# Kernel tuning notes

Hardware: AMD Instinct MI355X
Metric: run time of the kernel (lower is better)

The kernel has to match this reference:

```python
import jax, jax.numpy as jnp
import numpy as np

HID = 256
POS_FREQ = 10
DIR_FREQ = 4
POS_ENC = 3 * (2 * POS_FREQ + 1)   # 63
DIR_ENC = 3 * (2 * DIR_FREQ + 1)   # 27
N_PTS = 262144


def _posenc(x, num_freq):
    freqs = (2.0 ** jnp.arange(num_freq)).astype(x.dtype)      # [F]
    xf = x[..., None, :] * freqs[:, None]                       # [..., F, D]
    sc = jnp.stack([jnp.sin(xf), jnp.cos(xf)], axis=-2)         # [..., F, 2, D]
    return jnp.concatenate([x, sc.reshape(*x.shape[:-1], -1)], axis=-1)


def _linear_init(key, fan_in, fan_out):
    kw, kb = jax.random.split(key)
    s = 1.0 / np.sqrt(fan_in)
    W = jax.random.uniform(kw, (fan_in, fan_out), jnp.float32, -s, s)
    b = jax.random.uniform(kb, (fan_out,), jnp.float32, -s, s)
    return W, b


def setup_inputs() -> dict:
    key = jax.random.key(0)
    ks = jax.random.split(key, 16)
    inp = {
        "positions": jax.random.normal(ks[0], (N_PTS, 3), jnp.float32),
        "directions": jax.random.normal(ks[1], (N_PTS, 3), jnp.float32),
    }
    W, b = _linear_init(ks[2], POS_ENC, HID)
    inp["W_in"], inp["b_in"] = W, b
    # 7 hidden layers; layer index 4 takes skip concat (HID + POS_ENC)
    for i in range(7):
        fan_in = HID + POS_ENC if i == 4 else HID
        W, b = _linear_init(ks[3 + i], fan_in, HID)
        inp[f"W_h{i}"], inp[f"b_h{i}"] = W, b
    W, b = _linear_init(ks[10], HID, HID + 1)
    inp["W_out"], inp["b_out"] = W, b
    W, b = _linear_init(ks[11], HID + DIR_ENC, HID // 2)
    inp["W_r1"], inp["b_r1"] = W, b
    W, b = _linear_init(ks[12], HID // 2, 3)
    inp["W_r2"], inp["b_r2"] = W, b
    return inp


def _forward(positions, directions, W_in, b_in, hidden_params, W_out, b_out,
             W_r1, b_r1, W_r2, b_r2):
    pe = _posenc(positions, POS_FREQ)    # [N, 63]
    de = _posenc(directions, DIR_FREQ)   # [N, 27]
    h = jax.nn.relu(pe @ W_in + b_in)    # [N, 256]
    for i, (W, b) in enumerate(hidden_params):
        if i == 4:
            h = jnp.concatenate([h, pe], axis=-1)  # skip connection [N, 319]
        h = jax.nn.relu(h @ W + b)
    out = h @ W_out + b_out                      # [N, 257]
    features = out[..., :HID]                    # [N, 256]
    density = jax.nn.relu(out[..., HID:HID + 1])  # [N, 1]
    rgb_in = jnp.concatenate([features, de], axis=-1)  # [N, 283]
    rgb = jax.nn.sigmoid(jax.nn.relu(rgb_in @ W_r1 + b_r1) @ W_r2 + b_r2)  # [N, 3]
    return rgb, density


def reference(positions, directions, W_in, b_in,
              W_h0, b_h0, W_h1, b_h1, W_h2, b_h2, W_h3, b_h3,
              W_h4, b_h4, W_h5, b_h5, W_h6, b_h6,
              W_out, b_out, W_r1, b_r1, W_r2, b_r2):
    hidden = [(W_h0, b_h0), (W_h1, b_h1), (W_h2, b_h2), (W_h3, b_h3),
              (W_h4, b_h4), (W_h5, b_h5), (W_h6, b_h6)]
    return _forward(positions, directions, W_in, b_in, hidden,
                    W_out, b_out, W_r1, b_r1, W_r2, b_r2)
```

## Files before the change

kernel.cpp:

```cpp
#include <hip/hip_runtime.h>
#include <math.h>

#define NPTS 262144
#define MT 128

typedef __attribute__((ext_vector_type(8))) short bf16x8;
typedef __attribute__((ext_vector_type(4))) float f32x4;
typedef __attribute__((ext_vector_type(16))) float f32x16;
typedef __attribute__((ext_vector_type(2))) unsigned int u32x2;

#if defined(__has_builtin)
#if __has_builtin(__builtin_amdgcn_cvt_pk_bf16_f32)
#define HAVE_CVT_PK_BF16 1
#endif
#endif

__device__ __forceinline__ short f2bf(float f) {
    union { float f; unsigned u; } v; v.f = f;
    unsigned r = v.u + 0x7fffu + ((v.u >> 16) & 1u);
    return (short)(r >> 16);
}
__device__ __forceinline__ unsigned pk2(float a, float b) {
#ifdef HAVE_CVT_PK_BF16
    auto r = __builtin_amdgcn_cvt_pk_bf16_f32(a, b);
    unsigned u; __builtin_memcpy(&u, &r, 4);
    return u;
#else
    return ((unsigned)(unsigned short)f2bf(a)) |
           ((unsigned)(unsigned short)f2bf(b) << 16);
#endif
}

__device__ __forceinline__ void barrier_lds() {
    asm volatile("s_waitcnt lgkmcnt(0)" ::: "memory");
    __builtin_amdgcn_s_barrier();
}

#define OFF_IN   0
#define SZ_IN    (64*256)
#define OFF_H0   (OFF_IN + SZ_IN)
#define SZ_H     (256*256)
#define OFF_H1   (OFF_H0 + SZ_H)
#define OFF_H2   (OFF_H1 + SZ_H)
#define OFF_H3   (OFF_H2 + SZ_H)
#define OFF_H4   (OFF_H3 + SZ_H)
#define SZ_H4    (320*256)
#define OFF_H5   (OFF_H4 + SZ_H4)
#define OFF_H6   (OFF_H5 + SZ_H)
#define OFF_OUT  (OFF_H6 + SZ_H)
#define SZ_OUTM  (256*256)
#define OFF_OUTD (OFF_OUT + SZ_OUTM)
#define SZ_OUTD  (256*16)
#define OFF_R1   (OFF_OUTD + SZ_OUTD)
#define SZ_R1    (288*128)
#define OFF_R2   (OFF_R1 + SZ_R1)
#define SZ_R2    (128*16)
#define WS_TOTAL (OFF_R2 + SZ_R2)

struct PrepP { const float* W[11]; short* ws; };

__global__ __launch_bounds__(256) void prep_all(PrepP pp) {
    int i = blockIdx.x * 256 + threadIdx.x;
    if (i >= WS_TOTAL) return;
    const int offs[13] = {OFF_IN, OFF_H0, OFF_H1, OFF_H2, OFF_H3, OFF_H4,
                          OFF_H5, OFF_H6, OFF_OUT, OFF_OUTD, OFF_R1, OFF_R2,
                          WS_TOTAL};
    const int wsrc[12] = {0,1,2,3,4,5,6,7,8,8,9,10};
    const int Ks[12]   = {63,256,256,256,256,319,256,256,256,256,283,128};
    const int Nsrc[12] = {256,256,256,256,256,256,256,256,257,257,128,3};
    int seg = 0;
    while (i >= offs[seg + 1]) seg++;
    int li = i - offs[seg];
    int j = li & 7, L = (li >> 3) & 63, tile = li >> 9;
    const float* W = pp.W[wsrc[seg]];
    float v = 0.f;
    if (seg == 9) {
        int k = tile * 32 + ((L >> 4) << 3) + j;
        if (k < 256 && (L & 15) == 0) v = W[k * 257 + 256];
    } else if (seg == 11) {
        int k = tile * 32 + ((L >> 4) << 3) + j;
        int n = L & 15;
        if (k < 128 && n < 3) v = W[k * 3 + n];
    } else {
        int nNb = (seg == 10) ? 4 : 8;
        int nb = tile % nNb, kt = tile / nNb;
        int k = kt * 16 + ((L >> 5) << 3) + j;
        int n = nb * 32 + (L & 31);
        if (k < Ks[seg]) v = W[k * Nsrc[seg] + n];
    }
    pp.ws[i] = f2bf(v);
}

struct Params {
    const float *pos, *dir;
    const float *b_in, *b_h0, *b_h1, *b_h2, *b_h3, *b_h4, *b_h5, *b_h6;
    const float *b_out, *b_r1, *b_r2;
    const short *w;
    float *out;
};

template<int NKT, int NNB, int NS, int TM, int MODE>
__device__ __forceinline__ void layer32(const short* __restrict__ Wsw,
                                        const short* __restrict__ Wd,
                                        const float* __restrict__ bias,
                                        short* X, float* dout, int p0,
                                        int nbB, int mbB, int wave, int lane) {
    const int l31 = lane & 31, hi = lane >> 5;
    const short* xb = X + hi * 1024 + (mbB * 32 + l31) * 8;
    const short* wp = Wsw + (size_t)(nbB * 64 + lane) * 8;

    bf16x8 a0[NS], a1[NS];
#pragma unroll
    for (int s = 0; s < NS; s++)
        a0[s] = *(const bf16x8*)(wp + (size_t)s * 512);
#pragma unroll
    for (int s = 0; s < NS; s++)
        a1[s] = *(const bf16x8*)(wp + (size_t)(NNB + s) * 512);

    barrier_lds();

    if (MODE == 1) {
        const int l15 = lane & 15, quad = lane >> 4;
        const short* xd = X + quad * 1024 + (wave * 16 + l15) * 8;
        f32x4 ad = (f32x4){0.f, 0.f, 0.f, 0.f};
#pragma unroll
        for (int kt = 0; kt < 8; ++kt) {
            bf16x8 b = *(const bf16x8*)(xd + kt * 4096);
            bf16x8 a = *(const bf16x8*)(Wd + (size_t)(kt * 64 + lane) * 8);
            ad = __builtin_amdgcn_mfma_f32_16x16x32_bf16(a, b, ad, 0, 0, 0);
        }
        if (quad == 0)
            dout[3 * NPTS + p0 + wave * 16 + l15] = fmaxf(ad[0] + bias[256], 0.f);
    }

    f32x16 acc[NS][TM];
#pragma unroll
    for (int s = 0; s < NS; s++)
#pragma unroll
        for (int t = 0; t < TM; t++)
#pragma unroll
            for (int r = 0; r < 16; r++) acc[s][t][r] = 0.f;

    bf16x8 b_c[TM];
#pragma unroll
    for (int t = 0; t < TM; t++)
        b_c[t] = *(const bf16x8*)(xb + t * 256);

#pragma unroll
    for (int kt = 0; kt < NKT; ++kt) {
        bf16x8 b_n[TM], a_n[NS];
        if (kt + 1 < NKT) {
#pragma unroll
            for (int t = 0; t < TM; t++)
                b_n[t] = *(const bf16x8*)(xb + (kt + 1) * 2048 + t * 256);
        }
        if (kt + 2 < NKT) {
#pragma unroll
            for (int s = 0; s < NS; s++)
                a_n[s] = *(const bf16x8*)(wp + (size_t)((kt + 2) * NNB + s) * 512);
        }
        if ((kt & 1) == 0) {
#pragma unroll
            for (int s = 0; s < NS; s++)
#pragma unroll
                for (int t = 0; t < TM; t++)
                    acc[s][t] = __builtin_amdgcn_mfma_f32_32x32x16_bf16(a0[s], b_c[t], acc[s][t], 0, 0, 0);
        } else {
#pragma unroll
            for (int s = 0; s < NS; s++)
#pragma unroll
                for (int t = 0; t < TM; t++)
                    acc[s][t] = __builtin_amdgcn_mfma_f32_32x32x16_bf16(a1[s], b_c[t], acc[s][t], 0, 0, 0);
        }
        if (kt + 2 < NKT) {
            if ((kt & 1) == 0) {
#pragma unroll
                for (int s = 0; s < NS; s++) a0[s] = a_n[s];
            } else {
#pragma unroll
                for (int s = 0; s < NS; s++) a1[s] = a_n[s];
            }
        }
        if (kt + 1 < NKT) {
#pragma unroll
            for (int t = 0; t < TM; t++) b_c[t] = b_n[t];
        }
    }

    barrier_lds();

#pragma unroll
    for (int s = 0; s < NS; s++) {
        const int nb = nbB + s;
#pragma unroll
        for (int t = 0; t < TM; t++) {
            const int m = (mbB + t) * 32 + l31;
#pragma unroll
            for (int rq = 0; rq < 4; rq++) {
                const int nbase = nb * 32 + rq * 8 + hi * 4;
                const f32x4 bv = *(const f32x4*)(bias + nbase);
                float v0 = acc[s][t][rq * 4 + 0] + bv[0];
                float v1 = acc[s][t][rq * 4 + 1] + bv[1];
                float v2 = acc[s][t][rq * 4 + 2] + bv[2];
                float v3 = acc[s][t][rq * 4 + 3] + bv[3];
                if (MODE == 0) {
                    v0 = fmaxf(v0, 0.f); v1 = fmaxf(v1, 0.f);
                    v2 = fmaxf(v2, 0.f); v3 = fmaxf(v3, 0.f);
                }
                u32x2 w; w[0] = pk2(v0, v1); w[1] = pk2(v2, v3);
                *(u32x2*)(X + (size_t)(nb * 4 + rq) * 1024 + m * 8 + hi * 4) = w;
            }
        }
    }
}

__global__ __launch_bounds__(512, 4) void nerf_fused(Params P) {
    __shared__ __align__(16) short X[40 * 1024];
    const int tid = threadIdx.x;
    const int wave = tid >> 6, lane = tid & 63;
    const int p0 = blockIdx.x * MT;

    const int nbB_h = (wave & 3) * 2, mbB_h = (wave >> 2) * 2;

    for (int i = tid; i < 128 * 8; i += 512) {
        const int pt = i & 127, g = i >> 7;
        const float x0 = P.pos[(p0 + pt) * 3 + 0];
        const float x1 = P.pos[(p0 + pt) * 3 + 1];
        const float x2 = P.pos[(p0 + pt) * 3 + 2];
        bf16x8 v;
#pragma unroll
        for (int j = 0; j < 8; j++) {
            const int d = g * 8 + j;
            float val = 0.f;
            if (d < 3) val = (d == 0) ? x0 : (d == 1) ? x1 : x2;
            else if (d < 63) {
                const int e = d - 3, f = e / 6, r = e % 6;
                const float x = (r % 3 == 0) ? x0 : (r % 3 == 1) ? x1 : x2;
                const float xf = x * (float)(1 << f);
                val = (r < 3) ? sinf(xf) : cosf(xf);
            }
            v[j] = f2bf(val);
        }
        *(bf16x8*)(X + ((size_t)g * 128 + pt) * 8) = v;
        *(bf16x8*)(X + ((size_t)(32 + g) * 128 + pt) * 8) = v;
    }

    layer32< 4, 8, 2, 2, 0>(P.w + OFF_IN, nullptr, P.b_in, X, P.out, p0, nbB_h, mbB_h, wave, lane);
    layer32<16, 8, 2, 2, 0>(P.w + OFF_H0, nullptr, P.b_h0, X, P.out, p0, nbB_h, mbB_h, wave, lane);
    layer32<16, 8, 2, 2, 0>(P.w + OFF_H1, nullptr, P.b_h1, X, P.out, p0, nbB_h, mbB_h, wave, lane);
    layer32<16, 8, 2, 2, 0>(P.w + OFF_H2, nullptr, P.b_h2, X, P.out, p0, nbB_h, mbB_h, wave, lane);
    layer32<16, 8, 2, 2, 0>(P.w + OFF_H3, nullptr, P.b_h3, X, P.out, p0, nbB_h, mbB_h, wave, lane);
    layer32<20, 8, 2, 2, 0>(P.w + OFF_H4, nullptr, P.b_h4, X, P.out, p0, nbB_h, mbB_h, wave, lane);

    {
        const int ptD = tid & 127, gD = tid >> 7;
        const float x0 = P.dir[(p0 + ptD) * 3 + 0];
        const float x1 = P.dir[(p0 + ptD) * 3 + 1];
        const float x2 = P.dir[(p0 + ptD) * 3 + 2];
        bf16x8 de_v;
#pragma unroll
        for (int j = 0; j < 8; j++) {
            const int d = gD * 8 + j;
            float val = 0.f;
            if (d < 3) val = (d == 0) ? x0 : (d == 1) ? x1 : x2;
            else if (d < 27) {
                const int e = d - 3, f = e / 6, r = e % 6;
                const float x = (r % 3 == 0) ? x0 : (r % 3 == 1) ? x1 : x2;
                const float xf = x * (float)(1 << f);
                val = (r < 3) ? sinf(xf) : cosf(xf);
            }
            de_v[j] = f2bf(val);
        }
        *(bf16x8*)(X + ((size_t)(32 + gD) * 128 + ptD) * 8) = de_v;
    }

    layer32<16, 8, 2, 2, 0>(P.w + OFF_H5, nullptr, P.b_h5, X, P.out, p0, nbB_h, mbB_h, wave, lane);
    layer32<16, 8, 2, 2, 0>(P.w + OFF_H6, nullptr, P.b_h6, X, P.out, p0, nbB_h, mbB_h, wave, lane);
    layer32<16, 8, 2, 2, 1>(P.w + OFF_OUT, P.w + OFF_OUTD, P.b_out, X, P.out, p0, nbB_h, mbB_h, wave, lane);

    layer32<18, 4, 2, 1, 0>(P.w + OFF_R1, nullptr, P.b_r1, X, P.out, p0, (wave & 1) * 2, wave >> 1, wave, lane);

    barrier_lds();
    {
        const int l15 = lane & 15, quad = lane >> 4;
        const short* xb = X + quad * 1024 + (wave * 16 + l15) * 8;
        bf16x8 a0 = *(const bf16x8*)(P.w + OFF_R2 + (size_t)(0 * 64 + lane) * 8);
        bf16x8 a1 = *(const bf16x8*)(P.w + OFF_R2 + (size_t)(1 * 64 + lane) * 8);
        bf16x8 a2 = *(const bf16x8*)(P.w + OFF_R2 + (size_t)(2 * 64 + lane) * 8);
        bf16x8 a3 = *(const bf16x8*)(P.w + OFF_R2 + (size_t)(3 * 64 + lane) * 8);
        f32x4 acc = (f32x4){0.f, 0.f, 0.f, 0.f};
        bf16x8 b0 = *(const bf16x8*)(xb);
        bf16x8 b1 = *(const bf16x8*)(xb + 4096);
        bf16x8 b2 = *(const bf16x8*)(xb + 8192);
        bf16x8 b3 = *(const bf16x8*)(xb + 12288);
        acc = __builtin_amdgcn_mfma_f32_16x16x32_bf16(a0, b0, acc, 0, 0, 0);
        acc = __builtin_amdgcn_mfma_f32_16x16x32_bf16(a1, b1, acc, 0, 0, 0);
        acc = __builtin_amdgcn_mfma_f32_16x16x32_bf16(a2, b2, acc, 0, 0, 0);
        acc = __builtin_amdgcn_mfma_f32_16x16x32_bf16(a3, b3, acc, 0, 0, 0);
        if (quad == 0) {
#pragma unroll
            for (int r = 0; r < 3; r++) {
                const float v = acc[r] + P.b_r2[r];
                P.out[(size_t)(p0 + wave * 16 + l15) * 3 + r] = 1.f / (1.f + expf(-v));
            }
        }
    }
}

extern "C" void kernel_launch(void* const* d_in, const int* in_sizes, int n_in,
                              void* d_out, int out_size, void* d_ws, size_t ws_size,
                              hipStream_t stream) {
    short* ws = (short*)d_ws;

    PrepP pp;
    pp.W[0]  = (const float*)d_in[2];
    pp.W[1]  = (const float*)d_in[4];
    pp.W[2]  = (const float*)d_in[6];
    pp.W[3]  = (const float*)d_in[8];
    pp.W[4]  = (const float*)d_in[10];
    pp.W[5]  = (const float*)d_in[12];
    pp.W[6]  = (const float*)d_in[14];
    pp.W[7]  = (const float*)d_in[16];
    pp.W[8]  = (const float*)d_in[18];
    pp.W[9]  = (const float*)d_in[20];
    pp.W[10] = (const float*)d_in[22];
    pp.ws = ws;
    hipLaunchKernelGGL(prep_all, dim3((WS_TOTAL + 255) / 256), dim3(256), 0, stream, pp);

    Params P;
    P.pos  = (const float*)d_in[0];
    P.dir  = (const float*)d_in[1];
    P.b_in = (const float*)d_in[3];
    P.b_h0 = (const float*)d_in[5];
    P.b_h1 = (const float*)d_in[7];
    P.b_h2 = (const float*)d_in[9];
    P.b_h3 = (const float*)d_in[11];
    P.b_h4 = (const float*)d_in[13];
    P.b_h5 = (const float*)d_in[15];
    P.b_h6 = (const float*)d_in[17];
    P.b_out = (const float*)d_in[19];
    P.b_r1 = (const float*)d_in[21];
    P.b_r2 = (const float*)d_in[23];
    P.w = ws;
    P.out = (float*)d_out;
    hipLaunchKernelGGL(nerf_fused, dim3(NPTS / MT), dim3(512), 0, stream, P);
}
```

Baseline: 416.8 us.

## Halve block to 4 waves with each wave covering all 128 rows

```diff
diff --git a/kernel.cpp b/kernel.cpp
--- a/kernel.cpp
+++ b/kernel.cpp
@@ -121,16 +121,20 @@
 
     if (MODE == 1) {
         const int l15 = lane & 15, quad = lane >> 4;
-        const short* xd = X + quad * 1024 + (wave * 16 + l15) * 8;
-        f32x4 ad = (f32x4){0.f, 0.f, 0.f, 0.f};
-#pragma unroll
-        for (int kt = 0; kt < 8; ++kt) {
-            bf16x8 b = *(const bf16x8*)(xd + kt * 4096);
-            bf16x8 a = *(const bf16x8*)(Wd + (size_t)(kt * 64 + lane) * 8);
-            ad = __builtin_amdgcn_mfma_f32_16x16x32_bf16(a, b, ad, 0, 0, 0);
-        }
-        if (quad == 0)
-            dout[3 * NPTS + p0 + wave * 16 + l15] = fmaxf(ad[0] + bias[256], 0.f);
+#pragma unroll
+        for (int half = 0; half < 2; ++half) {
+            const int mt = wave * 2 + half;
+            const short* xd = X + quad * 1024 + (mt * 16 + l15) * 8;
+            f32x4 ad = (f32x4){0.f, 0.f, 0.f, 0.f};
+#pragma unroll
+            for (int kt = 0; kt < 8; ++kt) {
+                bf16x8 b = *(const bf16x8*)(xd + kt * 4096);
+                bf16x8 a = *(const bf16x8*)(Wd + (size_t)(kt * 64 + lane) * 8);
+                ad = __builtin_amdgcn_mfma_f32_16x16x32_bf16(a, b, ad, 0, 0, 0);
+            }
+            if (quad == 0)
+                dout[3 * NPTS + p0 + mt * 16 + l15] = fmaxf(ad[0] + bias[256], 0.f);
+        }
     }
 
     f32x16 acc[NS][TM];
@@ -214,15 +218,13 @@
     }
 }
 
-__global__ __launch_bounds__(512, 4) void nerf_fused(Params P) {
+__global__ __launch_bounds__(256, 2) void nerf_fused(Params P) {
     __shared__ __align__(16) short X[40 * 1024];
     const int tid = threadIdx.x;
     const int wave = tid >> 6, lane = tid & 63;
     const int p0 = blockIdx.x * MT;
 
-    const int nbB_h = (wave & 3) * 2, mbB_h = (wave >> 2) * 2;
-
-    for (int i = tid; i < 128 * 8; i += 512) {
+    for (int i = tid; i < 128 * 8; i += 256) {
         const int pt = i & 127, g = i >> 7;
         const float x0 = P.pos[(p0 + pt) * 3 + 0];
         const float x1 = P.pos[(p0 + pt) * 3 + 1];
@@ -245,15 +247,16 @@
         *(bf16x8*)(X + ((size_t)(32 + g) * 128 + pt) * 8) = v;
     }
 
-    layer32< 4, 8, 2, 2, 0>(P.w + OFF_IN, nullptr, P.b_in, X, P.out, p0, nbB_h, mbB_h, wave, lane);
-    layer32<16, 8, 2, 2, 0>(P.w + OFF_H0, nullptr, P.b_h0, X, P.out, p0, nbB_h, mbB_h, wave, lane);
-    layer32<16, 8, 2, 2, 0>(P.w + OFF_H1, nullptr, P.b_h1, X, P.out, p0, nbB_h, mbB_h, wave, lane);
-    layer32<16, 8, 2, 2, 0>(P.w + OFF_H2, nullptr, P.b_h2, X, P.out, p0, nbB_h, mbB_h, wave, lane);
-    layer32<16, 8, 2, 2, 0>(P.w + OFF_H3, nullptr, P.b_h3, X, P.out, p0, nbB_h, mbB_h, wave, lane);
-    layer32<20, 8, 2, 2, 0>(P.w + OFF_H4, nullptr, P.b_h4, X, P.out, p0, nbB_h, mbB_h, wave, lane);
-
-    {
-        const int ptD = tid & 127, gD = tid >> 7;
+    const int nbB_h = wave * 2;
+    layer32< 4, 8, 2, 4, 0>(P.w + OFF_IN, nullptr, P.b_in, X, P.out, p0, nbB_h, 0, wave, lane);
+    layer32<16, 8, 2, 4, 0>(P.w + OFF_H0, nullptr, P.b_h0, X, P.out, p0, nbB_h, 0, wave, lane);
+    layer32<16, 8, 2, 4, 0>(P.w + OFF_H1, nullptr, P.b_h1, X, P.out, p0, nbB_h, 0, wave, lane);
+    layer32<16, 8, 2, 4, 0>(P.w + OFF_H2, nullptr, P.b_h2, X, P.out, p0, nbB_h, 0, wave, lane);
+    layer32<16, 8, 2, 4, 0>(P.w + OFF_H3, nullptr, P.b_h3, X, P.out, p0, nbB_h, 0, wave, lane);
+    layer32<20, 8, 2, 4, 0>(P.w + OFF_H4, nullptr, P.b_h4, X, P.out, p0, nbB_h, 0, wave, lane);
+
+    for (int i = tid; i < 128 * 4; i += 256) {
+        const int ptD = i & 127, gD = i >> 7;
         const float x0 = P.dir[(p0 + ptD) * 3 + 0];
         const float x1 = P.dir[(p0 + ptD) * 3 + 1];
         const float x2 = P.dir[(p0 + ptD) * 3 + 2];
@@ -274,34 +277,38 @@
         *(bf16x8*)(X + ((size_t)(32 + gD) * 128 + ptD) * 8) = de_v;
     }
 
-    layer32<16, 8, 2, 2, 0>(P.w + OFF_H5, nullptr, P.b_h5, X, P.out, p0, nbB_h, mbB_h, wave, lane);
-    layer32<16, 8, 2, 2, 0>(P.w + OFF_H6, nullptr, P.b_h6, X, P.out, p0, nbB_h, mbB_h, wave, lane);
-    layer32<16, 8, 2, 2, 1>(P.w + OFF_OUT, P.w + OFF_OUTD, P.b_out, X, P.out, p0, nbB_h, mbB_h, wave, lane);
-
-    layer32<18, 4, 2, 1, 0>(P.w + OFF_R1, nullptr, P.b_r1, X, P.out, p0, (wave & 1) * 2, wave >> 1, wave, lane);
+    layer32<16, 8, 2, 4, 0>(P.w + OFF_H5, nullptr, P.b_h5, X, P.out, p0, nbB_h, 0, wave, lane);
+    layer32<16, 8, 2, 4, 0>(P.w + OFF_H6, nullptr, P.b_h6, X, P.out, p0, nbB_h, 0, wave, lane);
+    layer32<16, 8, 2, 4, 1>(P.w + OFF_OUT, P.w + OFF_OUTD, P.b_out, X, P.out, p0, nbB_h, 0, wave, lane);
+
+    layer32<18, 4, 1, 4, 0>(P.w + OFF_R1, nullptr, P.b_r1, X, P.out, p0, wave, 0, wave, lane);
 
     barrier_lds();
     {
         const int l15 = lane & 15, quad = lane >> 4;
-        const short* xb = X + quad * 1024 + (wave * 16 + l15) * 8;
-        bf16x8 a0 = *(const bf16x8*)(P.w + OFF_R2 + (size_t)(0 * 64 + lane) * 8);
-        bf16x8 a1 = *(const bf16x8*)(P.w + OFF_R2 + (size_t)(1 * 64 + lane) * 8);
-        bf16x8 a2 = *(const bf16x8*)(P.w + OFF_R2 + (size_t)(2 * 64 + lane) * 8);
-        bf16x8 a3 = *(const bf16x8*)(P.w + OFF_R2 + (size_t)(3 * 64 + lane) * 8);
-        f32x4 acc = (f32x4){0.f, 0.f, 0.f, 0.f};
-        bf16x8 b0 = *(const bf16x8*)(xb);
-        bf16x8 b1 = *(const bf16x8*)(xb + 4096);
-        bf16x8 b2 = *(const bf16x8*)(xb + 8192);
-        bf16x8 b3 = *(const bf16x8*)(xb + 12288);
-        acc = __builtin_amdgcn_mfma_f32_16x16x32_bf16(a0, b0, acc, 0, 0, 0);
-        acc = __builtin_amdgcn_mfma_f32_16x16x32_bf16(a1, b1, acc, 0, 0, 0);
-        acc = __builtin_amdgcn_mfma_f32_16x16x32_bf16(a2, b2, acc, 0, 0, 0);
-        acc = __builtin_amdgcn_mfma_f32_16x16x32_bf16(a3, b3, acc, 0, 0, 0);
-        if (quad == 0) {
-#pragma unroll
-            for (int r = 0; r < 3; r++) {
-                const float v = acc[r] + P.b_r2[r];
-                P.out[(size_t)(p0 + wave * 16 + l15) * 3 + r] = 1.f / (1.f + expf(-v));
+#pragma unroll
+        for (int half = 0; half < 2; ++half) {
+            const int mt = wave * 2 + half;
+            const short* xb = X + quad * 1024 + (mt * 16 + l15) * 8;
+            bf16x8 a0 = *(const bf16x8*)(P.w + OFF_R2 + (size_t)(0 * 64 + lane) * 8);
+            bf16x8 a1 = *(const bf16x8*)(P.w + OFF_R2 + (size_t)(1 * 64 + lane) * 8);
+            bf16x8 a2 = *(const bf16x8*)(P.w + OFF_R2 + (size_t)(2 * 64 + lane) * 8);
+            bf16x8 a3 = *(const bf16x8*)(P.w + OFF_R2 + (size_t)(3 * 64 + lane) * 8);
+            f32x4 acc = (f32x4){0.f, 0.f, 0.f, 0.f};
+            bf16x8 b0 = *(const bf16x8*)(xb);
+            bf16x8 b1 = *(const bf16x8*)(xb + 4096);
+            bf16x8 b2 = *(const bf16x8*)(xb + 8192);
+            bf16x8 b3 = *(const bf16x8*)(xb + 12288);
+            acc = __builtin_amdgcn_mfma_f32_16x16x32_bf16(a0, b0, acc, 0, 0, 0);
+            acc = __builtin_amdgcn_mfma_f32_16x16x32_bf16(a1, b1, acc, 0, 0, 0);
+            acc = __builtin_amdgcn_mfma_f32_16x16x32_bf16(a2, b2, acc, 0, 0, 0);
+            acc = __builtin_amdgcn_mfma_f32_16x16x32_bf16(a3, b3, acc, 0, 0, 0);
+            if (quad == 0) {
+#pragma unroll
+                for (int r = 0; r < 3; r++) {
+                    const float v = acc[r] + P.b_r2[r];
+                    P.out[(size_t)(p0 + mt * 16 + l15) * 3 + r] = 1.f / (1.f + expf(-v));
+                }
             }
         }
     }
@@ -343,5 +350,5 @@
     P.b_r2 = (const float*)d_in[23];
     P.w = ws;
     P.out = (float*)d_out;
-    hipLaunchKernelGGL(nerf_fused, dim3(NPTS / MT), dim3(512), 0, stream, P);
-}
+    hipLaunchKernelGGL(nerf_fused, dim3(NPTS / MT), dim3(256), 0, stream, P);
+}
```

New measurement: 457.6 us. 1.1x slower.
